# Kernel optimization log

Measured on AMD Instinct MI355X. Metric: run time of the kernel, lower is better.

## Reference

```python
import jax, jax.numpy as jnp
import numpy as np

B, N, C = 128, 8732, 21  # batch, SSD priors, VOC classes (incl. background)
EPS = 1e-7


def setup_inputs() -> dict:
    key = jax.random.key(0)
    k1, k2, k3 = jax.random.split(key, 3)
    return {
        "lam": jnp.float32(0.7),
        "conf": jax.random.uniform(k1, (B, N, C), dtype=jnp.float32),
        "conf_shuffle": jax.random.uniform(k2, (B, N, C), dtype=jnp.float32),
        "conf_interpolation": jax.random.uniform(k3, (B, N, C), dtype=jnp.float32),
    }


def reference(lam, conf, conf_shuffle, conf_interpolation):
    half = conf.shape[0] // 2
    # swap the two halves of the shuffled batch
    conf_temp = jnp.concatenate([conf_shuffle[half:], conf_shuffle[:half]], axis=0)

    # foreground mask: max class score beats background score, on both sides
    left_mask = jnp.max(conf[..., 1:], axis=-1) > conf[..., 0]
    right_mask = jnp.max(conf_temp[..., 1:], axis=-1) > conf_temp[..., 0]
    mask = (left_mask & right_mask).astype(conf.dtype)  # [B, N]

    mixed = lam * conf + (1.0 - lam) * conf_temp + EPS
    inter = conf_interpolation + EPS

    sg = jax.lax.stop_gradient
    # KLDivLoss(log_input, target) = target * (log(target) - log_input), summed over classes
    inter_t = sg(inter)
    kl_a = jnp.sum(inter_t * (jnp.log(inter_t) - jnp.log(mixed)), axis=-1)  # [B, N]
    mixed_t = sg(mixed)
    kl_b = jnp.sum(mixed_t * (jnp.log(mixed_t) - jnp.log(inter)), axis=-1)  # [B, N]

    cnt = jnp.sum(mask)
    # masked mean over selected (b, n) samples; 0 if mask empty
    loss = jnp.sum((kl_a + kl_b) * mask) / jnp.maximum(cnt, 1.0)
    return jnp.where(cnt > 0, loss / 2.0, jnp.float32(0.0))
```

## Files before the change

### kernel.cpp

```cpp
#include <hip/hip_runtime.h>


#define EPS 1e-7f

constexpr int B = 128;
constexpr int N = 8732;
constexpr int C = 21;
constexpr int ROWS = B * N;
constexpr int ELEMS = ROWS * C;
constexpr int HALF_ELEMS = (B / 2) * N * C;
constexpr int GELEMS = 63;
constexpr int NGROUPS = (ROWS + 2) / 3;
constexpr int BLOCK = 256;
constexpr int GRID = 2048;
constexpr int NWAVES = GRID * (BLOCK / 64);

__global__ __launch_bounds__(BLOCK, 4) void isd_main_kernel(
    const float* __restrict__ lam_p,
    const float* __restrict__ conf,
    const float* __restrict__ csh,
    const float* __restrict__ cin,
    double* __restrict__ partials)
{
    const int tid  = threadIdx.x;
    const int lane = tid & 63;
    const int wid  = __builtin_amdgcn_readfirstlane(
                         blockIdx.x * (BLOCK / 64) + (tid >> 6));

    const int dr   = lane / 21;
    const int cpos = lane - dr * 21;
    const int gb   = dr * 21;
    const bool lane_ok = lane < GELEMS;

    const float lam = lam_p[0];
    const float oml = 1.0f - lam;

    double bs = 0.0;
    float  bc = 0.0f;

    auto body = [&](int g) {
        const int  e     = g * GELEMS + lane;
        const bool valid = lane_ok && (e < ELEMS);
        const int  ec    = valid ? e : 0;

        const float cv  = conf[ec];
        const float ivr = cin[ec];
        const int   e2  = ec + ((ec < HALF_ELEMS) ? HALF_ELEMS : -HALF_ELEMS);
        const float tv  = csh[e2];

        const float iv = ivr + EPS;
        const float mv = fmaf(lam, cv, oml * tv) + EPS;
        const float klt = (iv - mv) * (__logf(iv) - __logf(mv));

        const float c0 = __shfl(cv, gb, 64);
        const float t0 = __shfl(tv, gb, 64);
        const unsigned long long balc = __ballot(cv > c0);
        const unsigned long long balt = __ballot(tv > t0);
        const bool fg = (((balc >> gb) & 0x1FFFFFull) != 0ull) &&
                        (((balt >> gb) & 0x1FFFFFull) != 0ull);

        const float m = (fg && valid) ? 1.0f : 0.0f;
        bs += (double)(klt * m);
        bc += (cpos == 0) ? m : 0.0f;
    };

    for (int g = wid; g < NGROUPS; g += 4 * NWAVES) {
        body(g);
        body(g + 1 * NWAVES);
        body(g + 2 * NWAVES);
        body(g + 3 * NWAVES);
    }

    double bcD = (double)bc;
    #pragma unroll
    for (int off = 32; off > 0; off >>= 1) {
        bs  += __shfl_down(bs,  off, 64);
        bcD += __shfl_down(bcD, off, 64);
    }

    __shared__ double r_sum[BLOCK / 64];
    __shared__ double r_cnt[BLOCK / 64];
    const int wave = tid >> 6;
    if ((tid & 63) == 0) { r_sum[wave] = bs; r_cnt[wave] = bcD; }
    __syncthreads();

    if (tid == 0) {
        double s = 0.0, c = 0.0;
        #pragma unroll
        for (int w = 0; w < BLOCK / 64; ++w) { s += r_sum[w]; c += r_cnt[w]; }
        partials[2 * blockIdx.x + 0] = s;
        partials[2 * blockIdx.x + 1] = c;
    }
}

__global__ __launch_bounds__(256) void isd_final_kernel(
    const double* __restrict__ partials,
    float* __restrict__ out)
{
    double s = 0.0, c = 0.0;
    for (int i = threadIdx.x; i < GRID; i += 256) {
        s += partials[2 * i + 0];
        c += partials[2 * i + 1];
    }
    #pragma unroll
    for (int off = 32; off > 0; off >>= 1) {
        s += __shfl_down(s, off, 64);
        c += __shfl_down(c, off, 64);
    }
    __shared__ double ss[4], sc[4];
    const int wave = threadIdx.x >> 6;
    const int lane = threadIdx.x & 63;
    if (lane == 0) { ss[wave] = s; sc[wave] = c; }
    __syncthreads();
    if (threadIdx.x == 0) {
        const double S  = ss[0] + ss[1] + ss[2] + ss[3];
        const double Cc = sc[0] + sc[1] + sc[2] + sc[3];
        out[0] = (Cc > 0.0) ? (float)(S / fmax(Cc, 1.0) * 0.5) : 0.0f;
    }
}

extern "C" void kernel_launch(void* const* d_in, const int* in_sizes, int n_in,
                              void* d_out, int out_size, void* d_ws, size_t ws_size,
                              hipStream_t stream) {
    const float* lam  = (const float*)d_in[0];
    const float* conf = (const float*)d_in[1];
    const float* csh  = (const float*)d_in[2];
    const float* cin  = (const float*)d_in[3];
    float* out = (float*)d_out;
    double* partials = (double*)d_ws;

    isd_main_kernel<<<GRID, BLOCK, 0, stream>>>(lam, conf, csh, cin, partials);
    isd_final_kernel<<<1, 256, 0, stream>>>(partials, out);
}
```

Before: 278.6 us.

## Vectorize loads to float4 per lane with double-buffered prefetch

Each lane now handles four consecutive elements through float4 loads over 252-element chunks (12 rows of 21 classes), replacing the old one-scalar-per-lane layout of 63 elements per wave. Because four elements can straddle two rows, per-lane row and background masks are precomputed. The foreground test uses paired shuffles and four ballots over lo/hi row segments. The grid-stride loop becomes a fixed 12-iteration unrolled loop with two register buffers and sched barriers, so the next chunk's loads are issued before the current one is computed. The aim is to raise effective memory bandwidth on this streaming reduction, at the cost of more register pressure and more complex mask logic.

After: 277.0 us. Within noise of the previous version (-0.6%).

```diff
diff --git a/kernel.cpp b/kernel.cpp
--- a/kernel.cpp
+++ b/kernel.cpp
@@ -6,14 +6,16 @@
 constexpr int B = 128;
 constexpr int N = 8732;
 constexpr int C = 21;
-constexpr int ROWS = B * N;
-constexpr int ELEMS = ROWS * C;
+constexpr int ELEMS = B * N * C;
 constexpr int HALF_ELEMS = (B / 2) * N * C;
-constexpr int GELEMS = 63;
-constexpr int NGROUPS = (ROWS + 2) / 3;
+constexpr int CHUNK = 252;
+constexpr int NCHUNKS = (ELEMS + CHUNK - 1) / CHUNK;
 constexpr int BLOCK = 256;
 constexpr int GRID = 2048;
 constexpr int NWAVES = GRID * (BLOCK / 64);
+constexpr int KPW = 12;
+
+typedef unsigned long long u64;
 
 __global__ __launch_bounds__(BLOCK, 4) void isd_main_kernel(
     const float* __restrict__ lam_p,
@@ -27,51 +29,127 @@
     const int wid  = __builtin_amdgcn_readfirstlane(
                          blockIdx.x * (BLOCK / 64) + (tid >> 6));
 
-    const int dr   = lane / 21;
-    const int cpos = lane - dr * 21;
-    const int gb   = dr * 21;
-    const bool lane_ok = lane < GELEMS;
+    const int  idx0    = 4 * lane;
+    const bool lane_ok = (lane < 63);
+    const int  r_lo = idx0 / 21;
+    const int  r_hi = (idx0 + 3) / 21;
+    const int  r1   = (idx0 + 1) / 21;
+    const int  r2   = (idx0 + 2) / 21;
+    const bool s1 = (r1 == r_lo), s2 = (r2 == r_lo), s3 = (r_hi == r_lo);
+    const bool t0 = (r_lo == r_hi), t1 = (r1 == r_hi), t2 = (r2 == r_hi);
+    const int  c0i = idx0 % 21, c1i = (idx0 + 1) % 21,
+               c2i = (idx0 + 2) % 21, c3i = (idx0 + 3) % 21;
+    const bool nz0 = (c0i != 0), nz1 = (c1i != 0), nz2 = (c2i != 0), nz3 = (c3i != 0);
+    const bool hj0 = !nz0, hj1 = !nz1, hj2 = !nz2, hj3 = !nz3;
+    const int  hl_lo = (21 * r_lo) >> 2;
+    const int  hl_hi = (21 * r_hi) >> 2;
+
+    auto rmask = [](int lo, int hi) -> u64 {
+        if (hi > 63) hi = 63;
+        if (lo > hi || lo > 63) return 0ull;
+        return ((1ull << (hi - lo + 1)) - 1ull) << lo;
+    };
+    const u64 mLL = rmask((21 * r_lo + 3) >> 2, (21 * r_lo + 20) >> 2);
+    const u64 mLH = rmask((21 * r_lo) >> 2,     (21 * r_lo + 17) >> 2);
+    const u64 mHL = rmask((21 * r_hi + 3) >> 2, (21 * r_hi + 20) >> 2);
+    const u64 mHH = rmask((21 * r_hi) >> 2,     (21 * r_hi + 17) >> 2);
 
     const float lam = lam_p[0];
     const float oml = 1.0f - lam;
 
-    double bs = 0.0;
-    float  bc = 0.0f;
-
-    auto body = [&](int g) {
-        const int  e     = g * GELEMS + lane;
-        const bool valid = lane_ok && (e < ELEMS);
-        const int  ec    = valid ? e : 0;
-
-        const float cv  = conf[ec];
-        const float ivr = cin[ec];
-        const int   e2  = ec + ((ec < HALF_ELEMS) ? HALF_ELEMS : -HALF_ELEMS);
-        const float tv  = csh[e2];
-
-        const float iv = ivr + EPS;
-        const float mv = fmaf(lam, cv, oml * tv) + EPS;
-        const float klt = (iv - mv) * (__logf(iv) - __logf(mv));
-
-        const float c0 = __shfl(cv, gb, 64);
-        const float t0 = __shfl(tv, gb, 64);
-        const unsigned long long balc = __ballot(cv > c0);
-        const unsigned long long balt = __ballot(tv > t0);
-        const bool fg = (((balc >> gb) & 0x1FFFFFull) != 0ull) &&
-                        (((balt >> gb) & 0x1FFFFFull) != 0ull);
-
-        const float m = (fg && valid) ? 1.0f : 0.0f;
-        bs += (double)(klt * m);
-        bc += (cpos == 0) ? m : 0.0f;
+    const float4* conf4 = (const float4*)conf;
+    const float4* csh4  = (const float4*)csh;
+    const float4* cin4  = (const float4*)cin;
+
+    double bs   = 0.0;
+    float  cntF = 0.0f;
+
+    auto issue = [&](int k, float4& cv4, float4& tv4, float4& iv4) {
+        const int  base = (wid + k * NWAVES) * CHUNK;
+        const int  e0   = base + idx0;
+        const bool vld  = lane_ok && (e0 < ELEMS);
+        const int  a    = vld ? e0 : 0;
+        const int  f    = a + ((a < HALF_ELEMS) ? HALF_ELEMS : -HALF_ELEMS);
+        cv4 = conf4[a >> 2];
+        iv4 = cin4 [a >> 2];
+        tv4 = csh4 [f >> 2];
     };
 
-    for (int g = wid; g < NGROUPS; g += 4 * NWAVES) {
-        body(g);
-        body(g + 1 * NWAVES);
-        body(g + 2 * NWAVES);
-        body(g + 3 * NWAVES);
-    }
-
-    double bcD = (double)bc;
+    auto compute = [&](int k, const float4& cv4, const float4& tv4, const float4& iv4) {
+        const int  e0   = (wid + k * NWAVES) * CHUNK + idx0;
+        const bool vld  = lane_ok && (e0 < ELEMS);
+        const float vldf = vld ? 1.0f : 0.0f;
+
+        const float headC = hj0 ? cv4.x : (hj1 ? cv4.y : (hj2 ? cv4.z : cv4.w));
+        const float headT = hj0 ? tv4.x : (hj1 ? tv4.y : (hj2 ? tv4.z : tv4.w));
+        const float c0lo = __shfl(headC, hl_lo, 64);
+        const float c0hi = __shfl(headC, hl_hi, 64);
+        const float t0lo = __shfl(headT, hl_lo, 64);
+        const float t0hi = __shfl(headT, hl_hi, 64);
+        const float cb0 = c0lo,                cb1 = s1 ? c0lo : c0hi,
+                    cb2 = s2 ? c0lo : c0hi,    cb3 = c0hi;
+        const float tb0 = t0lo,                tb1 = s1 ? t0lo : t0hi,
+                    tb2 = s2 ? t0lo : t0hi,    tb3 = t0hi;
+
+        const bool bC0 = vld && nz0 && (cv4.x > cb0);
+        const bool bC1 = vld && nz1 && (cv4.y > cb1);
+        const bool bC2 = vld && nz2 && (cv4.z > cb2);
+        const bool bC3 = vld && nz3 && (cv4.w > cb3);
+        const bool bT0 = vld && nz0 && (tv4.x > tb0);
+        const bool bT1 = vld && nz1 && (tv4.y > tb1);
+        const bool bT2 = vld && nz2 && (tv4.z > tb2);
+        const bool bT3 = vld && nz3 && (tv4.w > tb3);
+
+        const bool plC = bC0 | (s1 & bC1) | (s2 & bC2) | (s3 & bC3);
+        const bool phC = (t0 & bC0) | (t1 & bC1) | (t2 & bC2) | bC3;
+        const bool plT = bT0 | (s1 & bT1) | (s2 & bT2) | (s3 & bT3);
+        const bool phT = (t0 & bT0) | (t1 & bT1) | (t2 & bT2) | bT3;
+        const u64 blC = __ballot(plC);
+        const u64 bhC = __ballot(phC);
+        const u64 blT = __ballot(plT);
+        const u64 bhT = __ballot(phT);
+
+        const bool fgloC = ((blC & mLL) | (bhC & mLH)) != 0ull;
+        const bool fghiC = ((blC & mHL) | (bhC & mHH)) != 0ull;
+        const bool fgloT = ((blT & mLL) | (bhT & mLH)) != 0ull;
+        const bool fghiT = ((blT & mHL) | (bhT & mHH)) != 0ull;
+        const float mlo = (fgloC && fgloT) ? 1.0f : 0.0f;
+        const float mhi = (fghiC && fghiT) ? 1.0f : 0.0f;
+        const float m0 = mlo * vldf,               m1 = (s1 ? mlo : mhi) * vldf,
+                    m2 = (s2 ? mlo : mhi) * vldf,  m3 = mhi * vldf;
+
+        const float iv0 = iv4.x + EPS, iv1 = iv4.y + EPS,
+                    iv2 = iv4.z + EPS, iv3 = iv4.w + EPS;
+        const float mv0 = fmaf(lam, cv4.x, oml * tv4.x) + EPS;
+        const float mv1 = fmaf(lam, cv4.y, oml * tv4.y) + EPS;
+        const float mv2 = fmaf(lam, cv4.z, oml * tv4.z) + EPS;
+        const float mv3 = fmaf(lam, cv4.w, oml * tv4.w) + EPS;
+        const float kl0 = (iv0 - mv0) * (__logf(iv0) - __logf(mv0));
+        const float kl1 = (iv1 - mv1) * (__logf(iv1) - __logf(mv1));
+        const float kl2 = (iv2 - mv2) * (__logf(iv2) - __logf(mv2));
+        const float kl3 = (iv3 - mv3) * (__logf(iv3) - __logf(mv3));
+
+        bs += (double)(kl0 * m0);
+        bs += (double)(kl1 * m1);
+        bs += (double)(kl2 * m2);
+        bs += (double)(kl3 * m3);
+        cntF += (hj0 ? m0 : 0.0f) + (hj1 ? m1 : 0.0f)
+              + (hj2 ? m2 : 0.0f) + (hj3 ? m3 : 0.0f);
+    };
+
+    float4 cvA, tvA, ivA, cvB, tvB, ivB;
+    issue(0, cvA, tvA, ivA);
+    #pragma unroll
+    for (int k = 0; k < KPW; k += 2) {
+        issue(k + 1, cvB, tvB, ivB);
+        __builtin_amdgcn_sched_barrier(0);
+        compute(k, cvA, tvA, ivA);
+        issue(k + 2, cvA, tvA, ivA);
+        __builtin_amdgcn_sched_barrier(0);
+        compute(k + 1, cvB, tvB, ivB);
+    }
+
+    double bcD = (double)cntF;
     #pragma unroll
     for (int off = 32; off > 0; off >>= 1) {
         bs  += __shfl_down(bs,  off, 64);
```
